# Optimization experiments

Measured on AMD Instinct MI355X. Metric: run time of the kernel, lower is better.

The kernel has to match this reference:

```python
import jax, jax.numpy as jnp
import numpy as np

E, D, H, F = 1024, 64, 16, 4096  # embedding, per-head dim, heads, mlp hidden
B, S = 2, 2048
EPS = 1e-5


def _layernorm(x, g, b):
    m = jnp.mean(x, axis=-1, keepdims=True)
    v = jnp.mean((x - m) ** 2, axis=-1, keepdims=True)
    return (x - m) * jax.lax.rsqrt(v + EPS) * g + b


def setup_inputs() -> dict:
    key = jax.random.key(0)
    ks = jax.random.split(key, 12)
    s_e = 1.0 / np.sqrt(E)
    s_f = 1.0 / np.sqrt(F)
    return {
        "x": jax.random.normal(ks[0], (B, S, E), jnp.float32),
        "Wq": jax.random.normal(ks[1], (H, E, D), jnp.float32) * s_e,
        "bq": jnp.zeros((H, D), jnp.float32),
        "Wk": jax.random.normal(ks[2], (H, E, D), jnp.float32) * s_e,
        "bk": jnp.zeros((H, D), jnp.float32),
        "Wv": jax.random.normal(ks[3], (H, E, D), jnp.float32) * s_e,
        "bv": jnp.zeros((H, D), jnp.float32),
        "Wo": jax.random.normal(ks[4], (E, E), jnp.float32) * s_e,
        "bo": jnp.zeros((E,), jnp.float32),
        "ln1_g": jnp.ones((E,), jnp.float32),
        "ln1_b": jnp.zeros((E,), jnp.float32),
        "ln2_g": jnp.ones((E,), jnp.float32),
        "ln2_b": jnp.zeros((E,), jnp.float32),
        "W1": jax.random.normal(ks[5], (E, F), jnp.float32) * s_e,
        "b1": jnp.zeros((F,), jnp.float32),
        "W2": jax.random.normal(ks[6], (F, E), jnp.float32) * s_f,
        "b2": jnp.zeros((E,), jnp.float32),
    }


def reference(x, Wq, bq, Wk, bk, Wv, bv, Wo, bo, ln1_g, ln1_b, ln2_g, ln2_b, W1, b1, W2, b2):
    h = _layernorm(x, ln1_g, ln1_b)
    # batched-head projections: [H,B,S,D]
    q = jnp.einsum("bse,hed->hbsd", h, Wq) + bq[:, None, None, :]
    k = jnp.einsum("bse,hed->hbsd", h, Wk) + bk[:, None, None, :]
    v = jnp.einsum("bse,hed->hbsd", h, Wv) + bv[:, None, None, :]
    # faithful quirk: scores = K @ Q^T (no 1/sqrt(d)), softmax over query axis
    scores = jnp.einsum("hbsd,hbtd->hbst", k, q)  # [H,B,S_key,S_query]
    att = jax.nn.softmax(scores, axis=-1)
    o = jnp.einsum("hbst,hbtd->hbsd", att, v)  # [H,B,S,D]
    o = jnp.transpose(o, (1, 2, 0, 3)).reshape(x.shape[0], x.shape[1], -1)  # concat heads
    x = x + o @ Wo + bo
    m = _layernorm(x, ln2_g, ln2_b)
    m = jax.nn.relu(m @ W1 + b1) @ W2 + b2
    return x + m
```

## Files before the change

### kernel.cpp

```cpp
#include <hip/hip_runtime.h>
#include <cstdint>
#include <cstddef>

typedef __attribute__((ext_vector_type(8))) short short8;
typedef __attribute__((ext_vector_type(4))) float f32x4;
typedef __attribute__((ext_vector_type(4))) unsigned short ushort4v;

#define E_DIM 1024
#define D_DIM 64
#define H_DIM 16
#define F_DIM 4096
#define B_DIM 2
#define S_DIM 2048
#define M_DIM 4096
#define LN_EPS 1e-5f
#define LOG2E 1.4426950408889634f

__device__ __forceinline__ float bf2f(unsigned short u) {
  union { unsigned int i; float f; } v;
  v.i = ((unsigned int)u) << 16;
  return v.f;
}
__device__ __forceinline__ unsigned short f2bf(float f) {
  union { float f; unsigned int i; } v;
  v.f = f;
  unsigned int r = v.i + 0x7FFFu + ((v.i >> 16) & 1u);
  return (unsigned short)(r >> 16);
}
__device__ __forceinline__ unsigned int cvt_pk_bf16(float a, float b) {
  unsigned int r;
  asm("v_cvt_pk_bf16_f32 %0, %1, %2" : "=v"(r) : "v"(a), "v"(b));
  return r;
}
__device__ __forceinline__ float exp2_fast(float x) {
  float r;
  asm("v_exp_f32 %0, %1" : "=v"(r) : "v"(x));
  return r;
}

__device__ __forceinline__ void gload_lds16(const unsigned short* src,
                                            unsigned short* dst) {
  __builtin_amdgcn_global_load_lds(
      (const __attribute__((address_space(1))) void*)src,
      (__attribute__((address_space(3))) void*)dst, 16, 0, 0);
}

__global__ __launch_bounds__(256) void transpose_all(
    const float* __restrict__ Wq, const float* __restrict__ Wk,
    const float* __restrict__ Wv, const float* __restrict__ Wo,
    const float* __restrict__ W1, const float* __restrict__ W2,
    unsigned short* __restrict__ WqkvT, unsigned short* __restrict__ WoT,
    unsigned short* __restrict__ W1T, unsigned short* __restrict__ W2T) {
  int id = blockIdx.x;
  const float* in;
  unsigned short* out;
  int R, C;
  bool qkv = false;
  float scale = 1.f;
  if (id < 3072) {
    int seg = id >> 10;
    in = seg == 0 ? Wq : seg == 1 ? Wk : Wv;
    out = WqkvT + (size_t)seg * 1048576;
    R = 1024; C = 1024; qkv = true;
    if (seg == 0) scale = LOG2E;
    id &= 1023;
  } else if (id < 4096) {
    in = Wo; out = WoT; R = 1024; C = 1024; id -= 3072;
  } else if (id < 8192) {
    in = W1; out = W1T; R = 1024; C = 4096; id -= 4096;
  } else {
    in = W2; out = W2T; R = 4096; C = 1024; id -= 8192;
  }
  const int tpc = C >> 5;
  const int c0 = (id % tpc) * 32, r0 = (id / tpc) * 32;
  __shared__ float t[32][33];
  const int tid = threadIdx.x;
  {
    const int rr = tid >> 3, c4 = (tid & 7) * 4;
    size_t addr;
    if (qkv)
      addr = (size_t)(c0 >> 6) * 65536 + (size_t)(r0 + rr) * 64 +
             ((c0 & 63) + c4);
    else
      addr = (size_t)(r0 + rr) * C + (c0 + c4);
    float4 v = *(const float4*)(in + addr);
    t[rr][c4 + 0] = v.x;
    t[rr][c4 + 1] = v.y;
    t[rr][c4 + 2] = v.z;
    t[rr][c4 + 3] = v.w;
  }
  __syncthreads();
  {
    const int cc = tid >> 3, k4 = (tid & 7) * 4;
    ushort4v hi;
    hi.x = f2bf(t[k4 + 0][cc] * scale);
    hi.y = f2bf(t[k4 + 1][cc] * scale);
    hi.z = f2bf(t[k4 + 2][cc] * scale);
    hi.w = f2bf(t[k4 + 3][cc] * scale);
    *(ushort4v*)(out + (size_t)(c0 + cc) * R + (r0 + k4)) = hi;
  }
}

__global__ __launch_bounds__(256) void ln_kernel(const float* __restrict__ x,
                                                 const float* __restrict__ g,
                                                 const float* __restrict__ b,
                                                 unsigned short* __restrict__ o) {
  const int row = blockIdx.x;
  const float* xp = x + (size_t)row * E_DIM;
  const int t4 = threadIdx.x * 4;
  float4 xv = *(const float4*)(xp + t4);
  float s = xv.x + xv.y + xv.z + xv.w;
  float ss = xv.x * xv.x + xv.y * xv.y + xv.z * xv.z + xv.w * xv.w;
#pragma unroll
  for (int off = 32; off > 0; off >>= 1) {
    s += __shfl_down(s, off);
    ss += __shfl_down(ss, off);
  }
  __shared__ float red[8];
  const int wid = threadIdx.x >> 6;
  if ((threadIdx.x & 63) == 0) {
    red[wid] = s;
    red[4 + wid] = ss;
  }
  __syncthreads();
  if (threadIdx.x == 0) {
    float S = red[0] + red[1] + red[2] + red[3];
    float SS = red[4] + red[5] + red[6] + red[7];
    float mean = S * (1.0f / E_DIM);
    float var = SS * (1.0f / E_DIM) - mean * mean;
    red[0] = mean;
    red[1] = rsqrtf(var + LN_EPS);
  }
  __syncthreads();
  const float mean = red[0], rstd = red[1];
  float4 gv = *(const float4*)(g + t4);
  float4 bv = *(const float4*)(b + t4);
  ushort4v hi;
  hi.x = f2bf((xv.x - mean) * rstd * gv.x + bv.x);
  hi.y = f2bf((xv.y - mean) * rstd * gv.y + bv.y);
  hi.z = f2bf((xv.z - mean) * rstd * gv.z + bv.z);
  hi.w = f2bf((xv.w - mean) * rstd * gv.w + bv.w);
  *(ushort4v*)(o + (size_t)row * E_DIM + t4) = hi;
}

template <int MODE>
__global__ __launch_bounds__(256) void mfma_gemm(
    const unsigned short* __restrict__ A, const unsigned short* __restrict__ B,
    const float* __restrict__ bias, const float* __restrict__ bias2,
    const float* __restrict__ bias3, void* __restrict__ out0,
    void* __restrict__ out1, void* __restrict__ out2, int M, int N, int K) {
  __shared__ unsigned short As[8192];
  __shared__ unsigned short Bs[8192];
  const int tid = threadIdx.x;
  const int nwg = gridDim.x * gridDim.y;
  const int flat = blockIdx.y * gridDim.x + blockIdx.x;
  const int swz = (flat & 7) * (nwg >> 3) + (flat >> 3);
  const int m0 = (swz / gridDim.x) * 128, n0 = (swz % gridDim.x) * 128;
  const int lane = tid & 63, wid = tid >> 6;
  const int wr = wid >> 1, wc = wid & 1;
  const int lr = lane & 15, lg = lane >> 4;

  f32x4 acc[4][4];
#pragma unroll
  for (int i = 0; i < 4; ++i)
#pragma unroll
    for (int j = 0; j < 4; ++j) acc[i][j] = {0.f, 0.f, 0.f, 0.f};

  int kbeg = 0, kend = K;
  if constexpr (MODE == 4) {
    int kslice = K / gridDim.z;
    kbeg = blockIdx.z * kslice;
    kend = kbeg + kslice;
  }

  for (int k0 = kbeg; k0 < kend; k0 += 64) {
#pragma unroll
    for (int c = 0; c < 4; ++c) {
      int chunk = wid * 4 + c;
      int rb = chunk >> 1, kc = chunk & 1;
      size_t goff = (size_t)(rb * 16 + lr) * K + k0 + kc * 32 + lg * 8;
      gload_lds16(A + (size_t)m0 * K + goff, As + chunk * 512);
      gload_lds16(B + (size_t)n0 * K + goff, Bs + chunk * 512);
    }
    __syncthreads();
#pragma unroll
    for (int kc = 0; kc < 2; ++kc) {
      short8 af[4], bf[4];
#pragma unroll
      for (int mi = 0; mi < 4; ++mi)
        af[mi] = *(const short8*)(As + ((wr * 4 + mi) * 2 + kc) * 512 + lane * 8);
#pragma unroll
      for (int ni = 0; ni < 4; ++ni)
        bf[ni] = *(const short8*)(Bs + ((wc * 4 + ni) * 2 + kc) * 512 + lane * 8);
#pragma unroll
      for (int mi = 0; mi < 4; ++mi)
#pragma unroll
        for (int ni = 0; ni < 4; ++ni)
          acc[mi][ni] = __builtin_amdgcn_mfma_f32_16x16x32_bf16(
              af[mi], bf[ni], acc[mi][ni], 0, 0, 0);
    }
    __syncthreads();
  }
#pragma unroll
  for (int mi = 0; mi < 4; ++mi) {
#pragma unroll
    for (int ni = 0; ni < 4; ++ni) {
      int n = n0 + wc * 64 + ni * 16 + lr;
#pragma unroll
      for (int rr = 0; rr < 4; ++rr) {
        int m = m0 + wr * 64 + mi * 16 + lg * 4 + rr;
        float v = acc[mi][ni][rr];
        if constexpr (MODE == 0) {
          int seg = n >> 10, nn = n & 1023;
          const float* bp = seg == 0 ? bias : seg == 1 ? bias2 : bias3;
          v += (seg == 0) ? bp[nn] * LOG2E : bp[nn];
          int hh = nn >> 6, d = nn & 63, bb = m >> 11, srow = m & 2047;
          size_t pb = (size_t)(hh * 2 + bb) * 131072;
          if (seg == 0)
            ((unsigned short*)out0)[pb + (size_t)srow * 64 + d] = f2bf(v);
          else if (seg == 1)
            ((unsigned short*)out1)[pb + (size_t)srow * 64 + d] = f2bf(v);
          else
            ((unsigned short*)out2)[pb + (size_t)d * 2048 + srow] = f2bf(v);
        } else if constexpr (MODE == 3) {
          ((unsigned short*)out0)[(size_t)m * N + n] = f2bf(fmaxf(v + bias[n], 0.f));
        } else {
          unsafeAtomicAdd((float*)out0 + (size_t)m * N + n, v);
        }
      }
    }
  }
}

__global__ __launch_bounds__(256, 4) void attn_mfma(
    const unsigned short* __restrict__ Q, const unsigned short* __restrict__ K,
    const unsigned short* __restrict__ Vt, unsigned short* __restrict__ O) {
  __shared__ unsigned short Qs[2][4096];
  __shared__ unsigned short Vs[2][4096];
  const int bid = blockIdx.x;
  const int wg = (bid & 7) * 128 + (bid >> 3);
  const int pair = wg >> 5, stile = wg & 31;
  const int tid = threadIdx.x, lane = tid & 63, wid = tid >> 6;
  const int lr = lane & 15, lg = lane >> 4;
  const size_t pbase = (size_t)pair * 131072;

  const int s_own = stile * 64 + wid * 16 + lr;
  short8 kb[2];
#pragma unroll
  for (int c = 0; c < 2; ++c)
    kb[c] = *(const short8*)(K + pbase + (size_t)s_own * 64 + c * 32 + lg * 8);

  f32x4 oa[4];
#pragma unroll
  for (int i = 0; i < 4; ++i) oa[i] = {0.f, 0.f, 0.f, 0.f};
  float mrun = -3e38f, lrun = 0.f;

  auto stage = [&](int buf, int t0) {
#pragma unroll
    for (int c = 0; c < 2; ++c) {
      int chunk = wid * 2 + c;
      gload_lds16(Q + pbase + (size_t)(t0 + wid * 16 + lr) * 64 + c * 32 + lg * 8,
                  &Qs[buf][chunk * 512]);
      gload_lds16(Vt + pbase + (size_t)(wid * 16 + lr) * 2048 + t0 + c * 32 + lg * 8,
                  &Vs[buf][chunk * 512]);
    }
  };

  stage(0, 0);
  __syncthreads();

  for (int it = 0; it < 32; ++it) {
    const int cur = it & 1;
    if (it < 31) stage(cur ^ 1, (it + 1) * 64);

    f32x4 sacc[4];
#pragma unroll
    for (int j = 0; j < 4; ++j) {
      sacc[j] = {0.f, 0.f, 0.f, 0.f};
      __builtin_amdgcn_s_setprio(1);
#pragma unroll
      for (int c = 0; c < 2; ++c) {
        short8 aq = *(const short8*)(&Qs[cur][(j * 2 + c) * 512 + lane * 8]);
        sacc[j] = __builtin_amdgcn_mfma_f32_16x16x32_bf16(aq, kb[c], sacc[j], 0, 0, 0);
      }
      __builtin_amdgcn_s_setprio(0);
    }
    float tm = fmaxf(
        fmaxf(fmaxf(fmaxf(sacc[0][0], sacc[0][1]), fmaxf(sacc[0][2], sacc[0][3])),
              fmaxf(fmaxf(sacc[1][0], sacc[1][1]), fmaxf(sacc[1][2], sacc[1][3]))),
        fmaxf(fmaxf(fmaxf(sacc[2][0], sacc[2][1]), fmaxf(sacc[2][2], sacc[2][3])),
              fmaxf(fmaxf(sacc[3][0], sacc[3][1]), fmaxf(sacc[3][2], sacc[3][3]))));
    tm = fmaxf(tm, __shfl_xor(tm, 16));
    tm = fmaxf(tm, __shfl_xor(tm, 32));
    if (!__all(tm - mrun <= 11.0f)) {
      float mnew = fmaxf(mrun, tm);
      float sc = exp2_fast(mrun - mnew);
      mrun = mnew;
      lrun *= sc;
#pragma unroll
      for (int di = 0; di < 4; ++di) {
        f32x4 t = oa[di];
        t[0] *= sc; t[1] *= sc; t[2] *= sc; t[3] *= sc;
        oa[di] = t;
      }
    }
    float p[4][4];
#pragma unroll
    for (int j = 0; j < 4; ++j)
#pragma unroll
      for (int r = 0; r < 4; ++r) p[j][r] = exp2_fast(sacc[j][r] - mrun);
    float lsum = ((p[0][0] + p[0][1]) + (p[0][2] + p[0][3])) +
                 ((p[1][0] + p[1][1]) + (p[1][2] + p[1][3])) +
                 ((p[2][0] + p[2][1]) + (p[2][2] + p[2][3])) +
                 ((p[3][0] + p[3][1]) + (p[3][2] + p[3][3]));
    lsum += __shfl_xor(lsum, 16);
    lsum += __shfl_xor(lsum, 32);
    lrun += lsum;
    unsigned int pw[4][2];
#pragma unroll
    for (int j = 0; j < 4; ++j) {
      pw[j][0] = cvt_pk_bf16(p[j][0], p[j][1]);
      pw[j][1] = cvt_pk_bf16(p[j][2], p[j][3]);
    }
#pragma unroll
    for (int kc = 0; kc < 2; ++kc) {
      unsigned int bw[4];
#pragma unroll
      for (int mm = 0; mm < 4; ++mm) {
        int src = ((lg & 1) * 2 + (mm >> 1)) * 16 + lr;
        int lo = __shfl((int)pw[2 * kc][mm & 1], src, 64);
        int hi = __shfl((int)pw[2 * kc + 1][mm & 1], src, 64);
        bw[mm] = (lg & 2) ? (unsigned)hi : (unsigned)lo;
      }
      union { unsigned int u[4]; short8 s8; } pb;
      pb.u[0] = bw[0]; pb.u[1] = bw[1]; pb.u[2] = bw[2]; pb.u[3] = bw[3];
      __builtin_amdgcn_s_setprio(1);
#pragma unroll
      for (int di = 0; di < 4; ++di) {
        short8 vf = *(const short8*)(&Vs[cur][(di * 2 + kc) * 512 + lane * 8]);
        oa[di] = __builtin_amdgcn_mfma_f32_16x16x32_bf16(vf, pb.s8, oa[di], 0, 0, 0);
      }
      __builtin_amdgcn_s_setprio(0);
    }
    __syncthreads();
  }

  const float inv = 1.f / lrun;
  const int b = pair & 1, h = pair >> 1;
  unsigned short* op = O + ((size_t)(b * 2048 + s_own)) * 1024 + h * 64;
#pragma unroll
  for (int di = 0; di < 4; ++di) {
    unsigned int w0 = cvt_pk_bf16(oa[di][0] * inv, oa[di][1] * inv);
    unsigned int w1 = cvt_pk_bf16(oa[di][2] * inv, oa[di][3] * inv);
    *(unsigned int*)(op + di * 16 + lg * 4) = w0;
    *(unsigned int*)(op + di * 16 + lg * 4 + 2) = w1;
  }
}

__global__ __launch_bounds__(256) void init_acc(const float* __restrict__ resid,
                                                const float* __restrict__ bias,
                                                float* __restrict__ out) {
  int i = blockIdx.x * 256 + threadIdx.x;
  float4 v = ((const float4*)resid)[i];
  float4 bb = ((const float4*)bias)[i & 255];
  v.x += bb.x; v.y += bb.y; v.z += bb.z; v.w += bb.w;
  ((float4*)out)[i] = v;
}

extern "C" void kernel_launch(void* const* d_in, const int* in_sizes, int n_in,
                              void* d_out, int out_size, void* d_ws,
                              size_t ws_size, hipStream_t stream) {
  const float* x = (const float*)d_in[0];
  const float* Wq = (const float*)d_in[1];
  const float* bq = (const float*)d_in[2];
  const float* Wk = (const float*)d_in[3];
  const float* bk = (const float*)d_in[4];
  const float* Wv = (const float*)d_in[5];
  const float* bv = (const float*)d_in[6];
  const float* Wo = (const float*)d_in[7];
  const float* bo = (const float*)d_in[8];
  const float* ln1_g = (const float*)d_in[9];
  const float* ln1_b = (const float*)d_in[10];
  const float* ln2_g = (const float*)d_in[11];
  const float* ln2_b = (const float*)d_in[12];
  const float* W1 = (const float*)d_in[13];
  const float* b1 = (const float*)d_in[14];
  const float* W2 = (const float*)d_in[15];
  const float* b2 = (const float*)d_in[16];

  char* w = (char*)d_ws;
  const size_t MB = 1024 * 1024;
  unsigned short* WqkvT = (unsigned short*)(w + 0 * MB);
  unsigned short* WoT = (unsigned short*)(w + 6 * MB);
  unsigned short* W1T = (unsigned short*)(w + 8 * MB);
  unsigned short* W2T = (unsigned short*)(w + 16 * MB);
  unsigned short* h = (unsigned short*)(w + 24 * MB);
  unsigned short* Qb = (unsigned short*)(w + 32 * MB);
  unsigned short* Kb = (unsigned short*)(w + 40 * MB);
  unsigned short* Vt = (unsigned short*)(w + 48 * MB);
  unsigned short* Obuf = (unsigned short*)(w + 56 * MB);
  unsigned short* m1 = (unsigned short*)(w + 32 * MB);
  float* x2 = (float*)(w + 64 * MB);

  const dim3 blk(256);

  transpose_all<<<12288, blk, 0, stream>>>(Wq, Wk, Wv, Wo, W1, W2, WqkvT, WoT,
                                           W1T, W2T);

  ln_kernel<<<M_DIM, blk, 0, stream>>>(x, ln1_g, ln1_b, h);

  mfma_gemm<0><<<dim3(24, 32), blk, 0, stream>>>(h, WqkvT, bq, bk, bv, Qb, Kb,
                                                 Vt, M_DIM, 3072, 1024);

  attn_mfma<<<1024, blk, 0, stream>>>(Qb, Kb, Vt, Obuf);

  init_acc<<<4096, blk, 0, stream>>>(x, bo, x2);
  mfma_gemm<4><<<dim3(8, 32, 2), blk, 0, stream>>>(Obuf, WoT, nullptr, nullptr,
                                                   nullptr, x2, nullptr,
                                                   nullptr, M_DIM, 1024, 1024);

  ln_kernel<<<M_DIM, blk, 0, stream>>>(x2, ln2_g, ln2_b, h);

  mfma_gemm<3><<<dim3(32, 32), blk, 0, stream>>>(h, W1T, b1, nullptr, nullptr,
                                                 m1, nullptr, nullptr, M_DIM,
                                                 4096, 1024);

  init_acc<<<4096, blk, 0, stream>>>(x2, b2, (float*)d_out);
  mfma_gemm<4><<<dim3(8, 32, 4), blk, 0, stream>>>(
      m1, W2T, nullptr, nullptr, nullptr, (float*)d_out, nullptr, nullptr,
      M_DIM, 1024, 4096);
}
```

Baseline: 515.1 us.

## Replace atomic split-K with fused epilogue and partial-buffer reduction

The Wo projection drops split-K and its init kernel, and instead fuses bias and residual addition directly into the GEMM epilogue with plain stores. The W2 GEMM writes split-K partials to separate workspace slices instead of using float atomics. A new reduce kernel sums the partials with the residual and bias. The number of slices is chosen from the workspace size. This removes atomic contention and the init passes, but halves the Wo grid parallelism and adds extra partial-buffer traffic for W2.

```diff
diff --git a/kernel.cpp b/kernel.cpp
--- a/kernel.cpp
+++ b/kernel.cpp
@@ -147,8 +147,9 @@
 __global__ __launch_bounds__(256) void mfma_gemm(
     const unsigned short* __restrict__ A, const unsigned short* __restrict__ B,
     const float* __restrict__ bias, const float* __restrict__ bias2,
-    const float* __restrict__ bias3, void* __restrict__ out0,
-    void* __restrict__ out1, void* __restrict__ out2, int M, int N, int K) {
+    const float* __restrict__ bias3, const float* __restrict__ resid,
+    void* __restrict__ out0, void* __restrict__ out1, void* __restrict__ out2,
+    int M, int N, int K) {
   __shared__ unsigned short As[8192];
   __shared__ unsigned short Bs[8192];
   const int tid = threadIdx.x;
@@ -167,7 +168,7 @@
     for (int j = 0; j < 4; ++j) acc[i][j] = {0.f, 0.f, 0.f, 0.f};
 
   int kbeg = 0, kend = K;
-  if constexpr (MODE == 4) {
+  if constexpr (MODE == 5) {
     int kslice = K / gridDim.z;
     kbeg = blockIdx.z * kslice;
     kend = kbeg + kslice;
@@ -201,6 +202,9 @@
     }
     __syncthreads();
   }
+  float* part;
+  if constexpr (MODE == 5)
+    part = (float*)out0 + (size_t)blockIdx.z * M * N;
 #pragma unroll
   for (int mi = 0; mi < 4; ++mi) {
 #pragma unroll
@@ -222,10 +226,13 @@
             ((unsigned short*)out1)[pb + (size_t)srow * 64 + d] = f2bf(v);
           else
             ((unsigned short*)out2)[pb + (size_t)d * 2048 + srow] = f2bf(v);
+        } else if constexpr (MODE == 2) {
+          size_t ad = (size_t)m * N + n;
+          ((float*)out0)[ad] = v + bias[n] + resid[ad];
         } else if constexpr (MODE == 3) {
           ((unsigned short*)out0)[(size_t)m * N + n] = f2bf(fmaxf(v + bias[n], 0.f));
         } else {
-          unsafeAtomicAdd((float*)out0 + (size_t)m * N + n, v);
+          part[(size_t)m * N + n] = v;
         }
       }
     }
@@ -357,14 +364,23 @@
   }
 }
 
-__global__ __launch_bounds__(256) void init_acc(const float* __restrict__ resid,
-                                                const float* __restrict__ bias,
-                                                float* __restrict__ out) {
-  int i = blockIdx.x * 256 + threadIdx.x;
-  float4 v = ((const float4*)resid)[i];
-  float4 bb = ((const float4*)bias)[i & 255];
-  v.x += bb.x; v.y += bb.y; v.z += bb.z; v.w += bb.w;
-  ((float4*)out)[i] = v;
+__global__ __launch_bounds__(256) void reduce_out(const float* __restrict__ P,
+                                                  int nz,
+                                                  const float* __restrict__ x2,
+                                                  const float* __restrict__ b2,
+                                                  float* __restrict__ out) {
+#pragma unroll
+  for (int k = 0; k < 4; ++k) {
+    size_t idx = (size_t)blockIdx.x * 1024 + k * 256 + threadIdx.x;
+    float4 v = ((const float4*)x2)[idx];
+    float4 bb = ((const float4*)b2)[idx & 255];
+    v.x += bb.x; v.y += bb.y; v.z += bb.z; v.w += bb.w;
+    for (int z = 0; z < nz; ++z) {
+      float4 p = ((const float4*)P)[(size_t)z * 1048576 + idx];
+      v.x += p.x; v.y += p.y; v.z += p.z; v.w += p.w;
+    }
+    ((float4*)out)[idx] = v;
+  }
 }
 
 extern "C" void kernel_launch(void* const* d_in, const int* in_sizes, int n_in,
@@ -401,6 +417,9 @@
   unsigned short* Obuf = (unsigned short*)(w + 56 * MB);
   unsigned short* m1 = (unsigned short*)(w + 32 * MB);
   float* x2 = (float*)(w + 64 * MB);
+  float* Pz = (float*)(w + 80 * MB);
+
+  int nz = (ws_size >= 145 * MB) ? 4 : (ws_size >= 113 * MB) ? 2 : 1;
 
   const dim3 blk(256);
 
@@ -409,24 +428,24 @@
 
   ln_kernel<<<M_DIM, blk, 0, stream>>>(x, ln1_g, ln1_b, h);
 
-  mfma_gemm<0><<<dim3(24, 32), blk, 0, stream>>>(h, WqkvT, bq, bk, bv, Qb, Kb,
-                                                 Vt, M_DIM, 3072, 1024);
+  mfma_gemm<0><<<dim3(24, 32), blk, 0, stream>>>(h, WqkvT, bq, bk, bv, nullptr,
+                                                 Qb, Kb, Vt, M_DIM, 3072, 1024);
 
   attn_mfma<<<1024, blk, 0, stream>>>(Qb, Kb, Vt, Obuf);
 
-  init_acc<<<4096, blk, 0, stream>>>(x, bo, x2);
-  mfma_gemm<4><<<dim3(8, 32, 2), blk, 0, stream>>>(Obuf, WoT, nullptr, nullptr,
-                                                   nullptr, x2, nullptr,
-                                                   nullptr, M_DIM, 1024, 1024);
+  mfma_gemm<2><<<dim3(8, 32), blk, 0, stream>>>(Obuf, WoT, bo, nullptr, nullptr,
+                                                x, x2, nullptr, nullptr, M_DIM,
+                                                1024, 1024);
 
   ln_kernel<<<M_DIM, blk, 0, stream>>>(x2, ln2_g, ln2_b, h);
 
   mfma_gemm<3><<<dim3(32, 32), blk, 0, stream>>>(h, W1T, b1, nullptr, nullptr,
-                                                 m1, nullptr, nullptr, M_DIM,
-                                                 4096, 1024);
-
-  init_acc<<<4096, blk, 0, stream>>>(x2, b2, (float*)d_out);
-  mfma_gemm<4><<<dim3(8, 32, 4), blk, 0, stream>>>(
-      m1, W2T, nullptr, nullptr, nullptr, (float*)d_out, nullptr, nullptr,
-      M_DIM, 1024, 4096);
-}
+                                                 nullptr, m1, nullptr, nullptr,
+                                                 M_DIM, 4096, 1024);
+
+  mfma_gemm<5><<<dim3(8, 32, nz), blk, 0, stream>>>(
+      m1, W2T, nullptr, nullptr, nullptr, nullptr, Pz, nullptr, nullptr, M_DIM,
+      1024, 4096);
+
+  reduce_out<<<1024, blk, 0, stream>>>(Pz, nz, x2, b2, (float*)d_out);
+}
```

Result: faster. 474.6 us (-7.9%).
